# Kernel tuning notes

Measured on AMD Instinct MI355X. Metric: run time of the kernel, lower is better.

The kernel has to match this reference:

```python
import jax, jax.numpy as jnp
import numpy as np
import math

HID = 4096
SLOTS = 8
HEADS = 8
BD = 512  # bottleneck_dim
HD = BD // HEADS  # effective head dim = 64
B, S = 4, 4096


def setup_inputs() -> dict:
    key = jax.random.key(0)
    ks = jax.random.split(key, 8)
    std = 1.0 / math.sqrt(HID)
    return {
        "hidden_states": jax.random.normal(ks[0], (B, S, HID), dtype=jnp.float32),
        "attention_mask": jax.random.randint(ks[1], (B, S), 0, 2, dtype=jnp.int32),
        "memory_slots": jax.random.normal(ks[2], (SLOTS, HID), dtype=jnp.float32) * std,
        # torch nn.Linear weights are [out_features, in_features]
        "Wq": jax.random.normal(ks[3], (BD, HID), dtype=jnp.float32) * std,
        "Wk": jax.random.normal(ks[4], (BD, HID), dtype=jnp.float32) * std,
        "Wv": jax.random.normal(ks[5], (BD, HID), dtype=jnp.float32) * std,
        "Wo": jax.random.normal(ks[6], (HID, BD), dtype=jnp.float32) * (1.0 / math.sqrt(BD)),
    }


def reference(hidden_states, attention_mask, memory_slots, Wq, Wk, Wv, Wo):
    # Q from learnable slots (same for every batch element): [slots, BD]
    Q = memory_slots @ Wq.T
    Q = Q.reshape(SLOTS, HEADS, HD)                      # n h d
    # K/V from sequence: [b, s, BD] -> [b, s, h, d]
    K = jnp.einsum('bsi,oi->bso', hidden_states, Wk).reshape(B, S, HEADS, HD)
    V = jnp.einsum('bsi,oi->bso', hidden_states, Wv).reshape(B, S, HEADS, HD)
    # scores: [b, h, n, s]
    scores = jnp.einsum('nhd,bshd->bhns', Q, K) / jnp.sqrt(jnp.array(HD, scores_dtype := jnp.float32))
    mask = attention_mask[:, None, None, :]              # [b,1,1,s]
    scores = jnp.where(mask == 0, jnp.finfo(scores.dtype).min, scores)
    attn = jax.nn.softmax(scores, axis=-1)
    # output: [b, n, h, d] -> [b, n, BD]
    out = jnp.einsum('bhns,bshd->bnhd', attn, V).reshape(B, SLOTS, BD)
    # o_proj back to hidden_size
    return jnp.einsum('bnd,od->bno', out, Wo)            # [b, slots, HID]
```

## Files before the change

### kernel.cpp

```cpp
#include <hip/hip_runtime.h>
#include <math.h>

#define HID   4096
#define SLOTS 8
#define HEADS 8
#define BD    512
#define HD    64
#define BB    4
#define SS    4096
#define R64   64


__global__ void q_kernel(const float* __restrict__ ms, const float* __restrict__ Wq,
                         float* __restrict__ Q) {
  int w = (blockIdx.x * blockDim.x + threadIdx.x) >> 6;
  int lane = threadIdx.x & 63;
  if (w >= SLOTS * BD) return;
  int n = w >> 9, o = w & (BD - 1);
  const float* a = ms + n * HID;
  const float* b = Wq + (size_t)o * HID;
  float acc = 0.f;
  for (int i = lane; i < HID; i += 64) acc = fmaf(a[i], b[i], acc);
  #pragma unroll
  for (int off = 32; off; off >>= 1) acc += __shfl_down(acc, off, 64);
  if (lane == 0) Q[w] = acc;
}

__global__ void qw_kernel(const float* __restrict__ Q, const float* __restrict__ Wk,
                          float* __restrict__ QW) {
  int idx = blockIdx.x * blockDim.x + threadIdx.x;
  int r = idx >> 12, i = idx & (HID - 1);
  int h = r >> 3, n = r & 7;
  const float* q  = Q + n * BD + h * HD;
  const float* wk = Wk + (size_t)(h * HD) * HID + i;
  float acc = 0.f;
  #pragma unroll 8
  for (int d = 0; d < HD; ++d) acc = fmaf(q[d], wk[(size_t)d * HID], acc);
  QW[idx] = acc * 0.125f;
}

__global__ __launch_bounds__(256) void scores_kernel(const float* __restrict__ hs,
                                                     const float* __restrict__ QW,
                                                     float* __restrict__ sp) {
  __shared__ float As[64][68];
  __shared__ float Bs[64][68];
  int stile = blockIdx.x, ks = blockIdx.y, b = blockIdx.z;
  int tid = threadIdx.x;
  int tx = tid & 15, ty = tid >> 4;
  const float* hsb = hs + ((size_t)b * SS + stile * 64) * HID;
  float acc[4][4] = {};
  int kk = (tid & 15) * 4, row = tid >> 4;
  for (int k0 = ks * 1024; k0 < ks * 1024 + 1024; k0 += 64) {
    #pragma unroll
    for (int j = 0; j < 4; ++j) {
      int s = row + 16 * j;
      float4 v = *(const float4*)(hsb + (size_t)s * HID + k0 + kk);
      As[kk + 0][s] = v.x; As[kk + 1][s] = v.y; As[kk + 2][s] = v.z; As[kk + 3][s] = v.w;
      float4 u = *(const float4*)(QW + (size_t)s * HID + k0 + kk);
      Bs[kk + 0][s] = u.x; Bs[kk + 1][s] = u.y; Bs[kk + 2][s] = u.z; Bs[kk + 3][s] = u.w;
    }
    __syncthreads();
    #pragma unroll 8
    for (int k = 0; k < 64; ++k) {
      float4 a  = *(const float4*)&As[k][ty * 4];
      float4 bq = *(const float4*)&Bs[k][tx * 4];
      float av[4] = {a.x, a.y, a.z, a.w};
      float bv[4] = {bq.x, bq.y, bq.z, bq.w};
      #pragma unroll
      for (int si = 0; si < 4; ++si)
        #pragma unroll
        for (int ri = 0; ri < 4; ++ri)
          acc[si][ri] = fmaf(av[si], bv[ri], acc[si][ri]);
    }
    __syncthreads();
  }
  size_t base = (((size_t)ks * BB + b) * R64) * SS + stile * 64;
  #pragma unroll
  for (int ri = 0; ri < 4; ++ri) {
    float4 v = make_float4(acc[0][ri], acc[1][ri], acc[2][ri], acc[3][ri]);
    int r = tx * 4 + ri;
    *(float4*)(sp + base + (size_t)r * SS + ty * 4) = v;
  }
}

__global__ __launch_bounds__(256) void softmax_kernel(const float* __restrict__ sp,
                                                      const int* __restrict__ mask,
                                                      float* __restrict__ attn) {
  int br = blockIdx.x;
  int b = br >> 6;
  int tid = threadIdx.x;
  const int* mrow = mask + b * SS;
  float vals[16];
  float mx = -INFINITY;
  #pragma unroll
  for (int j = 0; j < 16; ++j) {
    int s = tid + j * 256;
    float v = sp[(size_t)(0 * 256 + br) * SS + s] + sp[(size_t)(1 * 256 + br) * SS + s]
            + sp[(size_t)(2 * 256 + br) * SS + s] + sp[(size_t)(3 * 256 + br) * SS + s];
    if (mrow[s] == 0) v = -INFINITY;
    vals[j] = v;
    mx = fmaxf(mx, v);
  }
  __shared__ float redm[4], reds[4];
  #pragma unroll
  for (int off = 32; off; off >>= 1) mx = fmaxf(mx, __shfl_down(mx, off, 64));
  if ((tid & 63) == 0) redm[tid >> 6] = mx;
  __syncthreads();
  mx = fmaxf(fmaxf(redm[0], redm[1]), fmaxf(redm[2], redm[3]));
  float sum = 0.f;
  #pragma unroll
  for (int j = 0; j < 16; ++j) { vals[j] = expf(vals[j] - mx); sum += vals[j]; }
  #pragma unroll
  for (int off = 32; off; off >>= 1) sum += __shfl_down(sum, off, 64);
  if ((tid & 63) == 0) reds[tid >> 6] = sum;
  __syncthreads();
  sum = reds[0] + reds[1] + reds[2] + reds[3];
  float inv = 1.f / sum;
  #pragma unroll
  for (int j = 0; j < 16; ++j)
    attn[(size_t)br * SS + tid + j * 256] = vals[j] * inv;
}

__global__ __launch_bounds__(256) void ctx_kernel(const float* __restrict__ attn,
                                                  const float* __restrict__ hs,
                                                  float* __restrict__ cp) {
  __shared__ float As[64][68];
  __shared__ float Bs[64][68];
  int itile = blockIdx.x, ks = blockIdx.y, b = blockIdx.z;
  int tid = threadIdx.x;
  int tx = tid & 15, ty = tid >> 4;
  const float* ab = attn + (size_t)b * R64 * SS;
  const float* hb = hs + (size_t)b * SS * HID + itile * 64;
  float acc[4][4] = {};
  int kk = (tid & 15) * 4, row = tid >> 4;
  for (int s0 = ks * 1024; s0 < ks * 1024 + 1024; s0 += 64) {
    #pragma unroll
    for (int j = 0; j < 4; ++j) {
      int r = row + 16 * j;
      float4 u = *(const float4*)(ab + (size_t)r * SS + s0 + kk);
      As[kk + 0][r] = u.x; As[kk + 1][r] = u.y; As[kk + 2][r] = u.z; As[kk + 3][r] = u.w;
      int sk = r;
      float4 v = *(const float4*)(hb + (size_t)(s0 + sk) * HID + kk);
      *(float4*)&Bs[sk][kk] = v;
    }
    __syncthreads();
    #pragma unroll 8
    for (int k = 0; k < 64; ++k) {
      float4 a  = *(const float4*)&As[k][ty * 4];
      float4 bq = *(const float4*)&Bs[k][tx * 4];
      float av[4] = {a.x, a.y, a.z, a.w};
      float bv[4] = {bq.x, bq.y, bq.z, bq.w};
      #pragma unroll
      for (int ri = 0; ri < 4; ++ri)
        #pragma unroll
        for (int ii = 0; ii < 4; ++ii)
          acc[ri][ii] = fmaf(av[ri], bv[ii], acc[ri][ii]);
    }
    __syncthreads();
  }
  size_t base = (((size_t)ks * BB + b) * R64) * HID + itile * 64;
  #pragma unroll
  for (int ri = 0; ri < 4; ++ri) {
    float4 v = make_float4(acc[ri][0], acc[ri][1], acc[ri][2], acc[ri][3]);
    int r = ty * 4 + ri;
    *(float4*)(cp + base + (size_t)r * HID + tx * 4) = v;
  }
}

__global__ void ctx_reduce_kernel(const float* __restrict__ cp, float* __restrict__ ctx) {
  int idx = blockIdx.x * blockDim.x + threadIdx.x;
  const size_t n = (size_t)BB * R64 * HID;
  ctx[idx] = cp[idx] + cp[idx + n] + cp[idx + 2 * n] + cp[idx + 3 * n];
}

__global__ void out_kernel(const float* __restrict__ ctx, const float* __restrict__ Wv,
                           float* __restrict__ out) {
  int w = (blockIdx.x * blockDim.x + threadIdx.x) >> 6;
  int lane = threadIdx.x & 63;
  if (w >= BB * SLOTS * BD) return;
  int b = w >> 12, n = (w >> 9) & 7, hd = w & 511, h = hd >> 6;
  const float* c  = ctx + ((size_t)b * R64 + h * 8 + n) * HID;
  const float* wv = Wv + (size_t)hd * HID;
  float acc = 0.f;
  for (int i = lane; i < HID; i += 64) acc = fmaf(c[i], wv[i], acc);
  #pragma unroll
  for (int off = 32; off; off >>= 1) acc += __shfl_down(acc, off, 64);
  if (lane == 0) out[w] = acc;
}

__global__ void final_kernel(const float* __restrict__ out, const float* __restrict__ Wo,
                             float* __restrict__ y) {
  int w = (blockIdx.x * blockDim.x + threadIdx.x) >> 6;
  int lane = threadIdx.x & 63;
  if (w >= BB * SLOTS * HID) return;
  int bn = w >> 12, o = w & 4095;
  const float* orow = out + bn * BD;
  const float* wo = Wo + (size_t)o * BD;
  float acc = 0.f;
  #pragma unroll
  for (int d = lane; d < BD; d += 64) acc = fmaf(orow[d], wo[d], acc);
  #pragma unroll
  for (int off = 32; off; off >>= 1) acc += __shfl_down(acc, off, 64);
  if (lane == 0) y[w] = acc;
}

extern "C" void kernel_launch(void* const* d_in, const int* in_sizes, int n_in,
                              void* d_out, int out_size, void* d_ws, size_t ws_size,
                              hipStream_t stream) {
  const float* hs   = (const float*)d_in[0];
  const int*   mask = (const int*)d_in[1];
  const float* ms   = (const float*)d_in[2];
  const float* Wq   = (const float*)d_in[3];
  const float* Wk   = (const float*)d_in[4];
  const float* Wv   = (const float*)d_in[5];
  const float* Wo   = (const float*)d_in[6];

  float* ws   = (float*)d_ws;
  float* Q    = ws;
  float* QW   = Q + 4096;
  float* sp   = QW + 262144;
  float* attn = sp + 4194304;
  float* ctx  = attn + 1048576;
  float* out  = ctx + 1048576;

  q_kernel<<<dim3((SLOTS * BD * 64) / 256), 256, 0, stream>>>(ms, Wq, Q);
  qw_kernel<<<dim3((R64 * HID) / 256), 256, 0, stream>>>(Q, Wk, QW);
  scores_kernel<<<dim3(64, 4, 4), 256, 0, stream>>>(hs, QW, sp);
  softmax_kernel<<<dim3(BB * R64), 256, 0, stream>>>(sp, mask, attn);
  float* cp = sp;
  ctx_kernel<<<dim3(64, 4, 4), 256, 0, stream>>>(attn, hs, cp);
  ctx_reduce_kernel<<<dim3(4096), 256, 0, stream>>>(cp, ctx);
  out_kernel<<<dim3(4096), 256, 0, stream>>>(ctx, Wv, out);
  final_kernel<<<dim3(32768), 256, 0, stream>>>(out, Wo, (float*)d_out);
}
```

Before: 670.8 us.

## Use bf16 MFMA for scores and context GEMMs, drop split-K reduction

Replaces the fp32 FMA tiled GEMMs for scores and context with bf16 MFMA kernels. The fp32 hidden states are converted to bf16 on the fly, and QW and the attention weights are stored as bf16. The split-K partials and the separate reduce kernel are removed, so each block loops over the full K with register prefetch. This targets compute-bound fp32 FMA work and extra partial-sum traffic, but it lowers precision to bf16 and launches fewer blocks (256 instead of 1024), which reduces parallelism.

```diff
diff --git a/kernel.cpp b/kernel.cpp
--- a/kernel.cpp
+++ b/kernel.cpp
@@ -9,7 +9,15 @@
 #define BB    4
 #define SS    4096
 #define R64   64
-
+#define LSTR  72
+
+typedef __attribute__((ext_vector_type(8))) short bf16x8;
+typedef __attribute__((ext_vector_type(4))) float f32x4;
+
+__device__ __forceinline__ unsigned short f2bf(float x) {
+  unsigned int u = __builtin_bit_cast(unsigned int, x);
+  return (unsigned short)((u + 0x7fffu + ((u >> 16) & 1u)) >> 16);
+}
 
 __global__ void q_kernel(const float* __restrict__ ms, const float* __restrict__ Wq,
                          float* __restrict__ Q) {
@@ -27,7 +35,7 @@
 }
 
 __global__ void qw_kernel(const float* __restrict__ Q, const float* __restrict__ Wk,
-                          float* __restrict__ QW) {
+                          unsigned short* __restrict__ QW) {
   int idx = blockIdx.x * blockDim.x + threadIdx.x;
   int r = idx >> 12, i = idx & (HID - 1);
   int h = r >> 3, n = r & 7;
@@ -36,67 +44,85 @@
   float acc = 0.f;
   #pragma unroll 8
   for (int d = 0; d < HD; ++d) acc = fmaf(q[d], wk[(size_t)d * HID], acc);
-  QW[idx] = acc * 0.125f;
-}
-
-__global__ __launch_bounds__(256) void scores_kernel(const float* __restrict__ hs,
-                                                     const float* __restrict__ QW,
-                                                     float* __restrict__ sp) {
-  __shared__ float As[64][68];
-  __shared__ float Bs[64][68];
-  int stile = blockIdx.x, ks = blockIdx.y, b = blockIdx.z;
-  int tid = threadIdx.x;
-  int tx = tid & 15, ty = tid >> 4;
-  const float* hsb = hs + ((size_t)b * SS + stile * 64) * HID;
-  float acc[4][4] = {};
-  int kk = (tid & 15) * 4, row = tid >> 4;
-  for (int k0 = ks * 1024; k0 < ks * 1024 + 1024; k0 += 64) {
-    #pragma unroll
-    for (int j = 0; j < 4; ++j) {
-      int s = row + 16 * j;
-      float4 v = *(const float4*)(hsb + (size_t)s * HID + k0 + kk);
-      As[kk + 0][s] = v.x; As[kk + 1][s] = v.y; As[kk + 2][s] = v.z; As[kk + 3][s] = v.w;
-      float4 u = *(const float4*)(QW + (size_t)s * HID + k0 + kk);
-      Bs[kk + 0][s] = u.x; Bs[kk + 1][s] = u.y; Bs[kk + 2][s] = u.z; Bs[kk + 3][s] = u.w;
-    }
-    __syncthreads();
-    #pragma unroll 8
-    for (int k = 0; k < 64; ++k) {
-      float4 a  = *(const float4*)&As[k][ty * 4];
-      float4 bq = *(const float4*)&Bs[k][tx * 4];
-      float av[4] = {a.x, a.y, a.z, a.w};
-      float bv[4] = {bq.x, bq.y, bq.z, bq.w};
+  QW[idx] = f2bf(acc * 0.125f);
+}
+
+__global__ __launch_bounds__(256) void scores_mfma(const float* __restrict__ hs,
+                                                   const unsigned short* __restrict__ QW,
+                                                   float* __restrict__ sp) {
+  __shared__ unsigned short As[64 * LSTR];
+  __shared__ unsigned short Bs[64 * LSTR];
+  const int stile = blockIdx.x, b = blockIdx.y;
+  const int tid = threadIdx.x;
+  const int wv = tid >> 6, lane = tid & 63;
+  const int quad = lane >> 4, l16 = lane & 15;
+  const int srow = tid >> 2, kc = (tid & 3) << 4;
+  const float* hsp = hs + ((size_t)(b * SS + stile * 64 + srow)) * HID + kc;
+  const unsigned short* qwp = QW + (size_t)srow * HID + kc;
+
+  f32x4 acc[4] = {};
+  float4 fa0 = *(const float4*)(hsp + 0);
+  float4 fa1 = *(const float4*)(hsp + 4);
+  float4 fa2 = *(const float4*)(hsp + 8);
+  float4 fa3 = *(const float4*)(hsp + 12);
+  uint4 qb0 = *(const uint4*)(qwp);
+  uint4 qb1 = *(const uint4*)(qwp + 8);
+
+  for (int c = 0; c < 64; ++c) {
+    __syncthreads();
+    union { unsigned short us[16]; uint4 q[2]; } u;
+    float f[16] = {fa0.x, fa0.y, fa0.z, fa0.w, fa1.x, fa1.y, fa1.z, fa1.w,
+                   fa2.x, fa2.y, fa2.z, fa2.w, fa3.x, fa3.y, fa3.z, fa3.w};
+    #pragma unroll
+    for (int j = 0; j < 16; ++j) u.us[j] = f2bf(f[j]);
+    *(uint4*)&As[srow * LSTR + kc]     = u.q[0];
+    *(uint4*)&As[srow * LSTR + kc + 8] = u.q[1];
+    *(uint4*)&Bs[srow * LSTR + kc]     = qb0;
+    *(uint4*)&Bs[srow * LSTR + kc + 8] = qb1;
+    __syncthreads();
+    if (c < 63) {
+      const float* p = hsp + (size_t)(c + 1) * 64;
+      fa0 = *(const float4*)(p + 0);
+      fa1 = *(const float4*)(p + 4);
+      fa2 = *(const float4*)(p + 8);
+      fa3 = *(const float4*)(p + 12);
+      const unsigned short* q = qwp + (size_t)(c + 1) * 64;
+      qb0 = *(const uint4*)(q);
+      qb1 = *(const uint4*)(q + 8);
+    }
+    #pragma unroll
+    for (int ks = 0; ks < 2; ++ks) {
+      bf16x8 bfrag = *(const bf16x8*)&Bs[(wv * 16 + l16) * LSTR + ks * 32 + quad * 8];
       #pragma unroll
-      for (int si = 0; si < 4; ++si)
-        #pragma unroll
-        for (int ri = 0; ri < 4; ++ri)
-          acc[si][ri] = fmaf(av[si], bv[ri], acc[si][ri]);
-    }
-    __syncthreads();
-  }
-  size_t base = (((size_t)ks * BB + b) * R64) * SS + stile * 64;
-  #pragma unroll
-  for (int ri = 0; ri < 4; ++ri) {
-    float4 v = make_float4(acc[0][ri], acc[1][ri], acc[2][ri], acc[3][ri]);
-    int r = tx * 4 + ri;
-    *(float4*)(sp + base + (size_t)r * SS + ty * 4) = v;
+      for (int mt = 0; mt < 4; ++mt) {
+        bf16x8 afrag = *(const bf16x8*)&As[(mt * 16 + l16) * LSTR + ks * 32 + quad * 8];
+        acc[mt] = __builtin_amdgcn_mfma_f32_16x16x32_bf16(afrag, bfrag, acc[mt], 0, 0, 0);
+      }
+    }
+  }
+  const int r = wv * 16 + l16;
+  #pragma unroll
+  for (int mt = 0; mt < 4; ++mt) {
+    int s = stile * 64 + mt * 16 + quad * 4;
+    float4 v = make_float4(acc[mt][0], acc[mt][1], acc[mt][2], acc[mt][3]);
+    *(float4*)(sp + ((size_t)(b * R64 + r)) * SS + s) = v;
   }
 }
 
 __global__ __launch_bounds__(256) void softmax_kernel(const float* __restrict__ sp,
                                                       const int* __restrict__ mask,
-                                                      float* __restrict__ attn) {
+                                                      unsigned short* __restrict__ attn) {
   int br = blockIdx.x;
   int b = br >> 6;
   int tid = threadIdx.x;
+  const float* row = sp + (size_t)br * SS;
   const int* mrow = mask + b * SS;
   float vals[16];
   float mx = -INFINITY;
   #pragma unroll
   for (int j = 0; j < 16; ++j) {
     int s = tid + j * 256;
-    float v = sp[(size_t)(0 * 256 + br) * SS + s] + sp[(size_t)(1 * 256 + br) * SS + s]
-            + sp[(size_t)(2 * 256 + br) * SS + s] + sp[(size_t)(3 * 256 + br) * SS + s];
+    float v = row[s];
     if (mrow[s] == 0) v = -INFINITY;
     vals[j] = v;
     mx = fmaxf(mx, v);
@@ -118,59 +144,75 @@
   float inv = 1.f / sum;
   #pragma unroll
   for (int j = 0; j < 16; ++j)
-    attn[(size_t)br * SS + tid + j * 256] = vals[j] * inv;
-}
-
-__global__ __launch_bounds__(256) void ctx_kernel(const float* __restrict__ attn,
-                                                  const float* __restrict__ hs,
-                                                  float* __restrict__ cp) {
-  __shared__ float As[64][68];
-  __shared__ float Bs[64][68];
-  int itile = blockIdx.x, ks = blockIdx.y, b = blockIdx.z;
-  int tid = threadIdx.x;
-  int tx = tid & 15, ty = tid >> 4;
-  const float* ab = attn + (size_t)b * R64 * SS;
-  const float* hb = hs + (size_t)b * SS * HID + itile * 64;
-  float acc[4][4] = {};
-  int kk = (tid & 15) * 4, row = tid >> 4;
-  for (int s0 = ks * 1024; s0 < ks * 1024 + 1024; s0 += 64) {
-    #pragma unroll
-    for (int j = 0; j < 4; ++j) {
-      int r = row + 16 * j;
-      float4 u = *(const float4*)(ab + (size_t)r * SS + s0 + kk);
-      As[kk + 0][r] = u.x; As[kk + 1][r] = u.y; As[kk + 2][r] = u.z; As[kk + 3][r] = u.w;
-      int sk = r;
-      float4 v = *(const float4*)(hb + (size_t)(s0 + sk) * HID + kk);
-      *(float4*)&Bs[sk][kk] = v;
-    }
-    __syncthreads();
-    #pragma unroll 8
-    for (int k = 0; k < 64; ++k) {
-      float4 a  = *(const float4*)&As[k][ty * 4];
-      float4 bq = *(const float4*)&Bs[k][tx * 4];
-      float av[4] = {a.x, a.y, a.z, a.w};
-      float bv[4] = {bq.x, bq.y, bq.z, bq.w};
+    attn[(size_t)br * SS + tid + j * 256] = f2bf(vals[j] * inv);
+}
+
+__global__ __launch_bounds__(256) void ctx_mfma(const unsigned short* __restrict__ attn,
+                                                const float* __restrict__ hs,
+                                                float* __restrict__ ctx) {
+  __shared__ unsigned short As[64 * LSTR];
+  __shared__ unsigned short Bs[64 * LSTR];
+  const int itile = blockIdx.x, b = blockIdx.y;
+  const int tid = threadIdx.x;
+  const int wv = tid >> 6, lane = tid & 63;
+  const int quad = lane >> 4, l16 = lane & 15;
+  const int arow = tid >> 2, asc = (tid & 3) << 4;
+  const unsigned short* ap = attn + ((size_t)(b * R64 + arow)) * SS + asc;
+  const int p = tid & 31, g = tid >> 5;
+  const float* bp0 = hs + ((size_t)(b * SS + 2 * p)) * HID + itile * 64 + g * 8;
+  const float* bp1 = bp0 + HID;
+
+  f32x4 acc[4] = {};
+  uint4 aa0 = *(const uint4*)(ap);
+  uint4 aa1 = *(const uint4*)(ap + 8);
+  float4 hb00 = *(const float4*)(bp0);
+  float4 hb01 = *(const float4*)(bp0 + 4);
+  float4 hb10 = *(const float4*)(bp1);
+  float4 hb11 = *(const float4*)(bp1 + 4);
+
+  for (int c = 0; c < 64; ++c) {
+    __syncthreads();
+    *(uint4*)&As[arow * LSTR + asc]     = aa0;
+    *(uint4*)&As[arow * LSTR + asc + 8] = aa1;
+    {
+      float lo[8] = {hb00.x, hb00.y, hb00.z, hb00.w, hb01.x, hb01.y, hb01.z, hb01.w};
+      float hi[8] = {hb10.x, hb10.y, hb10.z, hb10.w, hb11.x, hb11.y, hb11.z, hb11.w};
       #pragma unroll
-      for (int ri = 0; ri < 4; ++ri)
-        #pragma unroll
-        for (int ii = 0; ii < 4; ++ii)
-          acc[ri][ii] = fmaf(av[ri], bv[ii], acc[ri][ii]);
-    }
-    __syncthreads();
-  }
-  size_t base = (((size_t)ks * BB + b) * R64) * HID + itile * 64;
-  #pragma unroll
-  for (int ri = 0; ri < 4; ++ri) {
-    float4 v = make_float4(acc[ri][0], acc[ri][1], acc[ri][2], acc[ri][3]);
-    int r = ty * 4 + ri;
-    *(float4*)(cp + base + (size_t)r * HID + tx * 4) = v;
-  }
-}
-
-__global__ void ctx_reduce_kernel(const float* __restrict__ cp, float* __restrict__ ctx) {
-  int idx = blockIdx.x * blockDim.x + threadIdx.x;
-  const size_t n = (size_t)BB * R64 * HID;
-  ctx[idx] = cp[idx] + cp[idx + n] + cp[idx + 2 * n] + cp[idx + 3 * n];
+      for (int j = 0; j < 8; ++j) {
+        unsigned int v = (unsigned int)f2bf(lo[j]) | ((unsigned int)f2bf(hi[j]) << 16);
+        ((unsigned int*)Bs)[(g * 8 + j) * (LSTR / 2) + p] = v;
+      }
+    }
+    __syncthreads();
+    if (c < 63) {
+      const unsigned short* an = ap + (size_t)(c + 1) * 64;
+      aa0 = *(const uint4*)(an);
+      aa1 = *(const uint4*)(an + 8);
+      const float* bn0 = bp0 + (size_t)(c + 1) * 64 * HID;
+      const float* bn1 = bn0 + HID;
+      hb00 = *(const float4*)(bn0);
+      hb01 = *(const float4*)(bn0 + 4);
+      hb10 = *(const float4*)(bn1);
+      hb11 = *(const float4*)(bn1 + 4);
+    }
+    #pragma unroll
+    for (int ks = 0; ks < 2; ++ks) {
+      bf16x8 bfrag = *(const bf16x8*)&Bs[(wv * 16 + l16) * LSTR + ks * 32 + quad * 8];
+      #pragma unroll
+      for (int mt = 0; mt < 4; ++mt) {
+        bf16x8 afrag = *(const bf16x8*)&As[(mt * 16 + l16) * LSTR + ks * 32 + quad * 8];
+        acc[mt] = __builtin_amdgcn_mfma_f32_16x16x32_bf16(afrag, bfrag, acc[mt], 0, 0, 0);
+      }
+    }
+  }
+  const int i = itile * 64 + wv * 16 + l16;
+  #pragma unroll
+  for (int mt = 0; mt < 4; ++mt) {
+    int r0 = mt * 16 + quad * 4;
+    #pragma unroll
+    for (int j = 0; j < 4; ++j)
+      ctx[((size_t)(b * R64 + r0 + j)) * HID + i] = acc[mt][j];
+  }
 }
 
 __global__ void out_kernel(const float* __restrict__ ctx, const float* __restrict__ Wv,
@@ -215,21 +257,19 @@
   const float* Wv   = (const float*)d_in[5];
   const float* Wo   = (const float*)d_in[6];
 
-  float* ws   = (float*)d_ws;
-  float* Q    = ws;
-  float* QW   = Q + 4096;
-  float* sp   = QW + 262144;
-  float* attn = sp + 4194304;
-  float* ctx  = attn + 1048576;
-  float* out  = ctx + 1048576;
+  char* ws = (char*)d_ws;
+  float*          Q    = (float*)ws;                    ws += 4096 * 4;
+  unsigned short* QW   = (unsigned short*)ws;           ws += R64 * HID * 2;
+  float*          sp   = (float*)ws;                    ws += (size_t)BB * R64 * SS * 4;
+  unsigned short* attn = (unsigned short*)ws;           ws += (size_t)BB * R64 * SS * 2;
+  float*          ctx  = (float*)ws;                    ws += (size_t)BB * R64 * HID * 4;
+  float*          out  = (float*)ws;
 
   q_kernel<<<dim3((SLOTS * BD * 64) / 256), 256, 0, stream>>>(ms, Wq, Q);
   qw_kernel<<<dim3((R64 * HID) / 256), 256, 0, stream>>>(Q, Wk, QW);
-  scores_kernel<<<dim3(64, 4, 4), 256, 0, stream>>>(hs, QW, sp);
+  scores_mfma<<<dim3(64, 4), 256, 0, stream>>>(hs, QW, sp);
   softmax_kernel<<<dim3(BB * R64), 256, 0, stream>>>(sp, mask, attn);
-  float* cp = sp;
-  ctx_kernel<<<dim3(64, 4, 4), 256, 0, stream>>>(attn, hs, cp);
-  ctx_reduce_kernel<<<dim3(4096), 256, 0, stream>>>(cp, ctx);
+  ctx_mfma<<<dim3(64, 4), 256, 0, stream>>>(attn, hs, ctx);
   out_kernel<<<dim3(4096), 256, 0, stream>>>(ctx, Wv, out);
   final_kernel<<<dim3(32768), 256, 0, stream>>>(out, Wo, (float*)d_out);
 }
```

After: 580.3 us. 13.5% less time.
